# Kernel tuning notes

Hardware: AMD Instinct MI355X
Metric: run time of the kernel (lower is better)

The kernel has to match this reference:

```python
import jax, jax.numpy as jnp
import numpy as np

B, S, R, H = 32, 512, 49, 768


def setup_inputs() -> dict:
    key = jax.random.key(0)
    ks = jax.random.split(key, 32)
    rn = lambda i, shape, s=1.0: jax.random.normal(ks[i], shape, dtype=jnp.float32) * s
    W = 0.05  # weight init scale to keep tanh/softmax in a sane range
    return {
        'text_features': rn(0, (B, S, H)),
        'img_features': rn(1, (B, R, H)),
        't1_w': rn(2, (H, H), W), 't1_b': rn(3, (H,), W),
        'i1_w': rn(4, (H, H), W),
        'a1_w': rn(5, (2 * H,), W), 'a1_b': rn(6, (), W),
        't2_w': rn(7, (H, H), W),
        'i2_w': rn(8, (H, H), W), 'i2_b': rn(9, (H,), W),
        'a2_w': rn(10, (2 * H,), W), 'a2_b': rn(11, (), W),
        'gt_w': rn(12, (H, H), W), 'gt_b': rn(13, (H,), W),
        'gi_w': rn(14, (H, H), W), 'gi_b': rn(15, (H,), W),
        'gg_w': rn(16, (2 * H, 1), W), 'gg_b': rn(17, (1,), W),
        'ft_w': rn(18, (H, H), W),
        'fm_w': rn(19, (H, H), W), 'fm_b': rn(20, (H,), W),
        'fg_w': rn(21, (2 * H, 1), W), 'fg_b': rn(22, (1,), W),
        'fr_w': rn(23, (H, H), W), 'fr_b': rn(24, (H,), W),
    }


def reference(text_features, img_features, t1_w, t1_b, i1_w, a1_w, a1_b,
              t2_w, i2_w, i2_b, a2_w, a2_b, gt_w, gt_b, gi_w, gi_b,
              gg_w, gg_b, ft_w, fm_w, fm_b, fg_w, fg_b, fr_w, fr_b):
    H = text_features.shape[-1]
    # --- CoAttention, stage 1 (text attends over image regions) ---
    # tanh(concat) is elementwise and att_linear_1 is rank-1, so split the score:
    # score[b,s,r] = tanh(t1(x_s)) . a1[:H] + tanh(i1(y_r)) . a1[H:] + b
    t_sc = jnp.tanh(text_features @ t1_w + t1_b) @ a1_w[:H]          # (B,S)
    i_sc = jnp.tanh(img_features @ i1_w) @ a1_w[H:]                  # (B,R)
    visual_att = jax.nn.softmax(t_sc[:, :, None] + i_sc[:, None, :] + a1_b, axis=-1)  # (B,S,R)
    att_img = jnp.einsum('bsr,brh->bsh', visual_att, img_features)   # (B,S,H)
    # --- CoAttention, stage 2 (attended-image queries attend over text) ---
    # concat order is [img, text] -> a2[:H] pairs with img part
    q_sc = jnp.tanh(att_img @ i2_w + i2_b) @ a2_w[:H]                # (B,S)
    k_sc = jnp.tanh(text_features @ t2_w) @ a2_w[H:]                 # (B,S)
    textual_att = jax.nn.softmax(q_sc[:, :, None] + k_sc[:, None, :] + a2_b, axis=-1)  # (B,S,S)
    att_text = jnp.einsum('bij,bjh->bih', textual_att, text_features)  # (B,S,H)
    # --- GMF gated fusion ---
    new_img = jnp.tanh(att_img @ gi_w + gi_b)
    new_txt = jnp.tanh(att_text @ gt_w + gt_b)
    gate = jax.nn.sigmoid(jnp.concatenate([new_img, new_txt], axis=-1) @ gg_w + gg_b)  # (B,S,1)
    multimodal = gate * new_img + (1.0 - gate) * new_txt
    # --- filtration gate ---
    concat_feat = jnp.concatenate([text_features @ ft_w, multimodal @ fm_w + fm_b], axis=-1)
    fgate = jax.nn.sigmoid(concat_feat @ fg_w + fg_b)                # (B,S,1)
    return fgate * jnp.tanh(multimodal @ fr_w + fr_b)
```

## Files before the change

### kernel.cpp

```cpp
#include <hip/hip_runtime.h>
#include <hip/hip_bf16.h>
#include <math.h>

constexpr int BD = 32;
constexpr int SD = 512;
constexpr int RD = 49;
constexpr int HD = 768;
constexpr int MT = BD * SD;
constexpr int MI = BD * RD;
constexpr int NP = 6;
constexpr int MBT3 = MT / 256;
constexpr int MBI3 = 7;
constexpr int NB3 = 3;
constexpr int NWG3 = (MBT3 + MBI3) * NB3;
constexpr int NT3 = HD / 64;

typedef __bf16 bf16;
typedef __bf16 bf16x4 __attribute__((ext_vector_type(4)));
typedef __bf16 bf16x8 __attribute__((ext_vector_type(8)));
typedef float f32x4 __attribute__((ext_vector_type(4)));

#define GLOAD_LDS16(g, l) __builtin_amdgcn_global_load_lds( \
    (__attribute__((address_space(1))) void*)(g),           \
    (__attribute__((address_space(3))) void*)(l), 16, 0, 0)
#define BAR() __builtin_amdgcn_s_barrier()
#define SCHED_FENCE() __builtin_amdgcn_sched_barrier(0)
#define WAITV(n) asm volatile("s_waitcnt vmcnt(" #n ")" ::: "memory")

__device__ __forceinline__ float fast_tanh(float x) {
    const float e = __expf(2.f * x);
    return 1.f - 2.f / (e + 1.f);
}

__global__ __launch_bounds__(256) void prep_text(
    const float* __restrict__ text, const float* __restrict__ v_f,
    bf16* __restrict__ text_bf, float* __restrict__ s_txt)
{
    const int row = blockIdx.x * 4 + (threadIdx.x >> 6);
    const int lane = threadIdx.x & 63;
    const float* tr = text + (size_t)row * HD;
    bf16* tb = text_bf + (size_t)row * HD;
    float acc = 0.f;
    #pragma unroll
    for (int c = 0; c < 3; ++c) {
        const int o = c * 256 + lane * 4;
        const f32x4 x = *(const f32x4*)(tr + o);
        const f32x4 v = *(const f32x4*)(v_f + o);
        bf16x4 b; b[0] = (bf16)x[0]; b[1] = (bf16)x[1]; b[2] = (bf16)x[2]; b[3] = (bf16)x[3];
        *(bf16x4*)(tb + o) = b;
        acc += x[0] * v[0] + x[1] * v[1] + x[2] * v[2] + x[3] * v[3];
    }
    for (int off = 32; off; off >>= 1) acc += __shfl_xor(acc, off);
    if (lane == 0) s_txt[row] = acc;
}

__global__ __launch_bounds__(256) void prep_misc(
    const float* __restrict__ ft_w, const float* __restrict__ fm_w,
    const float* __restrict__ fm_b, const float* __restrict__ fg_w,
    float* __restrict__ v_f, float* __restrict__ v_m, float* __restrict__ c_m,
    const float* __restrict__ img, bf16* __restrict__ img_bf,
    const float* __restrict__ t2_w, const float* __restrict__ i1_w,
    bf16* __restrict__ wt_t, bf16* __restrict__ wt_i)
{
    __shared__ float tile[64][65];
    const int bid = blockIdx.x;
    if (bid < 385) {
        const int idx = bid * 4 + (threadIdx.x >> 6);
        const int lane = threadIdx.x & 63;
        const float* row; const float* vecp; float* outp;
        if (idx < HD)            { row = ft_w + (size_t)idx * HD;        vecp = fg_w;      outp = v_f + idx; }
        else if (idx < 2 * HD)   { row = fm_w + (size_t)(idx - HD) * HD; vecp = fg_w + HD; outp = v_m + (idx - HD); }
        else if (idx == 2 * HD)  { row = fm_b;                           vecp = fg_w + HD; outp = c_m; }
        else return;
        float acc = 0.f;
        #pragma unroll
        for (int i = 0; i < HD / 64; ++i) acc += row[lane + 64 * i] * vecp[lane + 64 * i];
        for (int off = 32; off; off >>= 1) acc += __shfl_xor(acc, off);
        if (lane == 0) *outp = acc;
    } else if (bid < 385 + 588) {
        const int i = (bid - 385) * 256 + threadIdx.x;
        const int n8 = BD * RD * HD / 8;
        if (i >= n8) return;
        const size_t o = (size_t)i * 8;
        const f32x4 x0 = *(const f32x4*)(img + o);
        const f32x4 x1 = *(const f32x4*)(img + o + 4);
        bf16x8 b;
        b[0]=(bf16)x0[0]; b[1]=(bf16)x0[1]; b[2]=(bf16)x0[2]; b[3]=(bf16)x0[3];
        b[4]=(bf16)x1[0]; b[5]=(bf16)x1[1]; b[6]=(bf16)x1[2]; b[7]=(bf16)x1[3];
        *(bf16x8*)(img_bf + o) = b;
    } else {
        const int idx2 = bid - (385 + 588);
        const int z = idx2 / 144, rem = idx2 % 144;
        const int bx = rem % 12, by = rem / 12;
        const float* W = z ? i1_w : t2_w;
        bf16* Wt = z ? wt_i : wt_t;
        const int k0 = bx * 64, n0 = by * 64;
        const int t = threadIdx.x;
        const int rb = t >> 6, c = t & 63;
        #pragma unroll
        for (int i = 0; i < 16; ++i) {
            const int r = rb + i * 4;
            tile[r][c] = W[(size_t)(k0 + r) * HD + n0 + c];
        }
        __syncthreads();
        #pragma unroll
        for (int i = 0; i < 16; ++i) {
            const int r = rb + i * 4;
            Wt[(size_t)(n0 + r) * HD + k0 + c] = (bf16)tile[c][r];
        }
    }
}

__global__ __launch_bounds__(512, 2) void gemm3(
    const bf16* __restrict__ Atext, const bf16* __restrict__ WtT,
    const float* __restrict__ vecT, float* __restrict__ partT,
    const bf16* __restrict__ Aimg, const bf16* __restrict__ WtI,
    const float* __restrict__ vecI, float* __restrict__ partI)
{
    __shared__ __align__(16) bf16 As[2 * 16384];
    __shared__ __align__(16) bf16 Bs[2 * 16384];

    const int bid = blockIdx.x;
    const int q = NWG3 / 8, r = NWG3 % 8;
    const int xcd = bid % 8, sidx = bid / 8;
    const int o = (xcd < r ? xcd * (q + 1) : r * (q + 1) + (xcd - r) * q) + sidx;
    const int mb = o / NB3, nb = o % NB3;

    const bool isT = mb < MBT3;
    const bf16* A    = isT ? Atext : Aimg;
    const bf16* Wt   = isT ? WtT : WtI;
    const float* vec = isT ? vecT : vecI;
    float* part      = isT ? partT : partI;
    const int m0 = (isT ? mb : mb - MBT3) * 256;
    const int n0 = nb * 256;

    const int t = threadIdx.x;
    const int w = t >> 6, lane = t & 63;
    const int quad = lane >> 4, l16 = lane & 15;
    const int wm_idx = w & 3, wn_idx = w >> 2;
    const int wm2 = wm_idx * 64, wn2 = wn_idx * 128;

    const bf16* Ag = A  + (size_t)(m0 + l16) * HD + quad * 8;
    const bf16* Bg = Wt + (size_t)(n0 + l16) * HD + quad * 8;

    f32x4 acc[4][8] = {};

#define STAGE3(tt, bb) {                                                     \
    const int kk = (tt) * 64;                                                \
    _Pragma("unroll")                                                        \
    for (int h = 0; h < 2; ++h) {                                            \
        _Pragma("unroll")                                                    \
        for (int j = 0; j < 2; ++j) {                                        \
            const int rc = 2 * w + j;                                        \
            GLOAD_LDS16(Ag + (size_t)rc * 16 * HD + kk + h * 32,             \
                        As + (bb) * 16384 + (h * 16 + rc) * 512);            \
            GLOAD_LDS16(Bg + (size_t)rc * 16 * HD + kk + h * 32,             \
                        Bs + (bb) * 16384 + (h * 16 + rc) * 512);            \
        }                                                                    \
    }                                                                        \
}

#define COMPUTE3(bb) {                                                       \
    _Pragma("unroll")                                                        \
    for (int h = 0; h < 2; ++h) {                                            \
        bf16x8 af[4], bg[8];                                                 \
        _Pragma("unroll")                                                    \
        for (int fi = 0; fi < 4; ++fi)                                       \
            af[fi] = *(const bf16x8*)(As + (bb) * 16384 +                    \
                       (h * 16 + wm_idx * 4 + fi) * 512 + lane * 8);         \
        _Pragma("unroll")                                                    \
        for (int fj = 0; fj < 8; ++fj)                                       \
            bg[fj] = *(const bf16x8*)(Bs + (bb) * 16384 +                    \
                       (h * 16 + wn_idx * 8 + fj) * 512 + lane * 8);         \
        _Pragma("unroll")                                                    \
        for (int fi = 0; fi < 4; ++fi)                                       \
            _Pragma("unroll")                                                \
            for (int fj = 0; fj < 8; ++fj)                                   \
                acc[fi][fj] = __builtin_amdgcn_mfma_f32_16x16x32_bf16(       \
                    af[fi], bg[fj], acc[fi][fj], 0, 0, 0);                   \
    }                                                                        \
}

    STAGE3(0, 0);
    for (int tt = 0; tt < NT3 - 1; ++tt) {
        STAGE3(tt + 1, (tt + 1) & 1);
        WAITV(8);
        BAR();
        SCHED_FENCE();
        COMPUTE3(tt & 1);
        SCHED_FENCE();
        BAR();
    }
    WAITV(0);
    BAR();
    SCHED_FENCE();
    COMPUTE3((NT3 - 1) & 1);

#undef STAGE3
#undef COMPUTE3

    float vv[8];
    #pragma unroll
    for (int fj = 0; fj < 8; ++fj) vv[fj] = vec[n0 + wn2 + fj * 16 + l16];

    #pragma unroll
    for (int fi = 0; fi < 4; ++fi) {
        #pragma unroll
        for (int reg = 0; reg < 4; ++reg) {
            float p = 0.f;
            #pragma unroll
            for (int fj = 0; fj < 8; ++fj)
                p += fast_tanh(acc[fi][fj][reg]) * vv[fj];
            p += __shfl_xor(p, 1);
            p += __shfl_xor(p, 2);
            p += __shfl_xor(p, 4);
            p += __shfl_xor(p, 8);
            if (l16 == 0) {
                const int row = m0 + wm2 + fi * 16 + quad * 4 + reg;
                part[(size_t)row * NP + nb * 2 + wn_idx] = p;
            }
        }
    }
}

__global__ __launch_bounds__(256) void wsum3(
    const float* __restrict__ k_part, const float* __restrict__ i_part,
    const bf16* __restrict__ text_bf, const float* __restrict__ img,
    float* __restrict__ at_part, float* __restrict__ aimg)
{
    __shared__ float S[SD];
    __shared__ float red[4];
    __shared__ float P2[2][96][8];
    const int bid = blockIdx.x;
    const int t = threadIdx.x;

    if (bid < 128) {
        const int b = bid >> 2, jq = bid & 3;
        for (int j = t; j < SD; j += 256) {
            const float* p = k_part + (size_t)(b * SD + j) * NP;
            S[j] = p[0] + p[1] + p[2] + p[3] + p[4] + p[5];
        }
        __syncthreads();
        float m = fmaxf(S[t], S[t + 256]);
        for (int off = 32; off; off >>= 1) m = fmaxf(m, __shfl_xor(m, off));
        if ((t & 63) == 0) red[t >> 6] = m;
        __syncthreads();
        m = fmaxf(fmaxf(red[0], red[1]), fmaxf(red[2], red[3]));
        const float e0 = __expf(S[t] - m), e1 = __expf(S[t + 256] - m);
        S[t] = e0; S[t + 256] = e1;
        float lsum = e0 + e1;
        for (int off = 32; off; off >>= 1) lsum += __shfl_xor(lsum, off);
        __syncthreads();
        if ((t & 63) == 0) red[t >> 6] = lsum;
        __syncthreads();
        const float inv = 1.f / (red[0] + red[1] + red[2] + red[3]);
        const int o = t % 96, jh = t / 96;
        if (jh < 2) {
            float a[8] = {};
            const bf16* Xb = text_bf + ((size_t)b * SD + jq * 128 + jh * 64) * HD + o * 8;
            const float* Sp = S + jq * 128 + jh * 64;
            #pragma unroll 8
            for (int jj = 0; jj < 64; ++jj) {
                const bf16x8 v = *(const bf16x8*)(Xb + (size_t)jj * HD);
                const float s = Sp[jj];
                #pragma unroll
                for (int e = 0; e < 8; ++e) a[e] += s * (float)v[e];
            }
            #pragma unroll
            for (int e = 0; e < 8; ++e) P2[jh][o][e] = a[e];
        }
        __syncthreads();
        if (t < 96) {
            float* dst = at_part + ((size_t)(b * 4 + jq)) * HD + t * 8;
            f32x4 o0, o1;
            #pragma unroll
            for (int e = 0; e < 4; ++e) o0[e] = (P2[0][t][e] + P2[1][t][e]) * inv;
            #pragma unroll
            for (int e = 0; e < 4; ++e) o1[e] = (P2[0][t][e + 4] + P2[1][t][e + 4]) * inv;
            *(f32x4*)dst = o0;
            *(f32x4*)(dst + 4) = o1;
        }
    } else {
        const int idx = bid - 128;
        const int b = idx & 31, hy = idx >> 5;
        if (t < 64) {
            float s0 = -1e30f;
            if (t < RD) {
                const float* p = i_part + (size_t)(b * RD + t) * NP;
                s0 = p[0] + p[1] + p[2] + p[3] + p[4] + p[5];
            }
            float m = s0;
            for (int off = 32; off; off >>= 1) m = fmaxf(m, __shfl_xor(m, off));
            float e = (t < RD) ? __expf(s0 - m) : 0.f;
            float lsum = e;
            for (int off = 32; off; off >>= 1) lsum += __shfl_xor(lsum, off);
            if (t < RD) S[t] = e;
            if (t == 0) red[0] = 1.f / lsum;
        }
        __syncthreads();
        const float inv = red[0];
        const int h = hy * 256 + t;
        const float* Xb = img + (size_t)b * RD * HD + h;
        float acc = 0.f;
        #pragma unroll 7
        for (int j = 0; j < RD; ++j) acc += S[j] * Xb[(size_t)j * HD];
        aimg[b * HD + h] = acc * inv;
    }
}

__global__ __launch_bounds__(256) void ni_nt3(
    const float* __restrict__ aimg, const float* __restrict__ at_part,
    const float* __restrict__ gi_w, const float* __restrict__ gi_b,
    const float* __restrict__ gt_w, const float* __restrict__ gt_b,
    float* __restrict__ ni, float* __restrict__ nt)
{
    const int b = blockIdx.x, n0 = blockIdx.y * 128, which = blockIdx.z;
    const float* W = which ? gt_w : gi_w;
    const float* bias = which ? gt_b : gi_b;
    float* Y = which ? nt : ni;

    __shared__ float Xs[HD];
    __shared__ float part[8][32][4];
    const int t = threadIdx.x;
    if (which) {
        for (int h = t; h < HD; h += 256)
            Xs[h] = at_part[((size_t)(b * 4 + 0)) * HD + h] + at_part[((size_t)(b * 4 + 1)) * HD + h]
                  + at_part[((size_t)(b * 4 + 2)) * HD + h] + at_part[((size_t)(b * 4 + 3)) * HD + h];
    } else {
        for (int h = t; h < HD; h += 256) Xs[h] = aimg[b * HD + h];
    }
    __syncthreads();
    const int lane32 = t & 31, kq = t >> 5;
    const int n = n0 + lane32 * 4;
    f32x4 acc = {0.f, 0.f, 0.f, 0.f};
    const float* Wp = W + (size_t)(kq * 96) * HD + n;
    #pragma unroll 4
    for (int k = 0; k < 96; ++k) {
        const f32x4 wv = *(const f32x4*)(Wp + (size_t)k * HD);
        const float x = Xs[kq * 96 + k];
        acc[0] += x * wv[0]; acc[1] += x * wv[1];
        acc[2] += x * wv[2]; acc[3] += x * wv[3];
    }
    *(f32x4*)&part[kq][lane32][0] = acc;
    __syncthreads();
    if (t < 128) {
        float s = 0.f;
        #pragma unroll
        for (int q2 = 0; q2 < 8; ++q2) s += part[q2][t >> 2][t & 3];
        Y[b * HD + n0 + t] = fast_tanh(s + bias[n0 + t]);
    }
}

__global__ __launch_bounds__(256) void gateT3(
    const float* __restrict__ ni, const float* __restrict__ nt,
    const float* __restrict__ gg_w, const float* __restrict__ gg_b,
    const float* __restrict__ v_m, const float* __restrict__ c_m,
    const float* __restrict__ fg_b,
    const float* __restrict__ fr_w, const float* __restrict__ fr_b,
    float* __restrict__ T, float* __restrict__ s_mm)
{
    const int b = blockIdx.x, n0 = blockIdx.y * 128, t = threadIdx.x;
    __shared__ float Mm[HD];
    __shared__ float part[8][32][4];
    __shared__ float red[4];
    __shared__ float gsh;

    float accg = 0.f;
    for (int n = t; n < HD; n += 256)
        accg += ni[b * HD + n] * gg_w[n] + nt[b * HD + n] * gg_w[HD + n];
    for (int off = 32; off; off >>= 1) accg += __shfl_xor(accg, off);
    if ((t & 63) == 0) red[t >> 6] = accg;
    __syncthreads();
    if (t == 0) gsh = 1.f / (1.f + expf(-(red[0] + red[1] + red[2] + red[3] + gg_b[0])));
    __syncthreads();
    const float g = gsh;
    float a2 = 0.f;
    for (int n = t; n < HD; n += 256) {
        const float m = g * ni[b * HD + n] + (1.f - g) * nt[b * HD + n];
        Mm[n] = m;
        a2 += m * v_m[n];
    }
    __syncthreads();
    const int lane32 = t & 31, kq = t >> 5;
    const int n = n0 + lane32 * 4;
    f32x4 acc = {0.f, 0.f, 0.f, 0.f};
    const float* Wp = fr_w + (size_t)(kq * 96) * HD + n;
    #pragma unroll 4
    for (int k = 0; k < 96; ++k) {
        const f32x4 wv = *(const f32x4*)(Wp + (size_t)k * HD);
        const float x = Mm[kq * 96 + k];
        acc[0] += x * wv[0]; acc[1] += x * wv[1];
        acc[2] += x * wv[2]; acc[3] += x * wv[3];
    }
    *(f32x4*)&part[kq][lane32][0] = acc;
    if (blockIdx.y == 0) {
        for (int off = 32; off; off >>= 1) a2 += __shfl_xor(a2, off);
        if ((t & 63) == 0) red[t >> 6] = a2;
    }
    __syncthreads();
    if (blockIdx.y == 0 && t == 0)
        s_mm[b] = red[0] + red[1] + red[2] + red[3] + *c_m + fg_b[0];
    if (t < 128) {
        float s = 0.f;
        #pragma unroll
        for (int q2 = 0; q2 < 8; ++q2) s += part[q2][t >> 2][t & 3];
        T[b * HD + n0 + t] = fast_tanh(s + fr_b[n0 + t]);
    }
}

__global__ __launch_bounds__(256) void out_kernel(const float* __restrict__ s_txt,
                                                  const float* __restrict__ s_mm,
                                                  const float* __restrict__ T,
                                                  float* __restrict__ out) {
    const size_t idx = ((size_t)blockIdx.x * 256 + threadIdx.x) * 4;
    const int h = (int)(idx % HD);
    const int bs = (int)(idx / HD);
    const int b = bs >> 9;
    float f = s_txt[bs] + s_mm[b];
    f = 1.f / (1.f + expf(-f));
    const float* Tp = T + b * HD + h;
    f32x4 o;
    o[0] = f * Tp[0]; o[1] = f * Tp[1]; o[2] = f * Tp[2]; o[3] = f * Tp[3];
    *(f32x4*)(out + idx) = o;
}

extern "C" void kernel_launch(void* const* d_in, const int* in_sizes, int n_in,
                              void* d_out, int out_size, void* d_ws, size_t ws_size,
                              hipStream_t stream) {
    const float* text = (const float*)d_in[0];
    const float* img  = (const float*)d_in[1];
    const float* i1_w = (const float*)d_in[4];
    const float* a1_w = (const float*)d_in[5];
    const float* t2_w = (const float*)d_in[7];
    const float* a2_w = (const float*)d_in[10];
    const float* gt_w = (const float*)d_in[12];
    const float* gt_b = (const float*)d_in[13];
    const float* gi_w = (const float*)d_in[14];
    const float* gi_b = (const float*)d_in[15];
    const float* gg_w = (const float*)d_in[16];
    const float* gg_b = (const float*)d_in[17];
    const float* ft_w = (const float*)d_in[18];
    const float* fm_w = (const float*)d_in[19];
    const float* fm_b = (const float*)d_in[20];
    const float* fg_w = (const float*)d_in[21];
    const float* fg_b = (const float*)d_in[22];
    const float* fr_w = (const float*)d_in[23];
    const float* fr_b = (const float*)d_in[24];
    float* out = (float*)d_out;

    float* sc_ = out;
    float* i_part  = sc_;
    float* k_part  = sc_ + 38400;
    float* aimg    = sc_ + 449600;
    float* v_f     = sc_ + 498752;
    float* v_m     = sc_ + 499520;
    float* c_m     = sc_ + 500288;
    float* at_part = sc_ + 500352;
    float* ni      = sc_ + 598656;
    float* nt      = sc_ + 623232;
    bf16* text_bf  = (bf16*)(sc_ + 672384);
    bf16* img_bf   = (bf16*)(sc_ + 6963840);
    bf16* wt_t     = (bf16*)(sc_ + 7565952);
    bf16* wt_i     = (bf16*)(sc_ + 7860864);

    float* ws    = (float*)d_ws;
    float* s_txt = ws;
    float* s_mm  = ws + 16384;
    float* T     = ws + 16448;

    prep_misc<<<dim3(385 + 588 + 288), dim3(256), 0, stream>>>(
        ft_w, fm_w, fm_b, fg_w, v_f, v_m, c_m, img, img_bf, t2_w, i1_w, wt_t, wt_i);
    prep_text<<<dim3(MT / 4), dim3(256), 0, stream>>>(text, v_f, text_bf, s_txt);
    gemm3<<<dim3(NWG3), dim3(512), 0, stream>>>(
        text_bf, wt_t, a2_w + HD, k_part, img_bf, wt_i, a1_w + HD, i_part);
    wsum3<<<dim3(224), dim3(256), 0, stream>>>(
        k_part, i_part, text_bf, img, at_part, aimg);
    ni_nt3<<<dim3(BD, 6, 2), dim3(256), 0, stream>>>(
        aimg, at_part, gi_w, gi_b, gt_w, gt_b, ni, nt);
    gateT3<<<dim3(BD, 6), dim3(256), 0, stream>>>(
        ni, nt, gg_w, gg_b, v_m, c_m, fg_b, fr_w, fr_b, T, s_mm);
    out_kernel<<<dim3((MT * HD / 4) / 256), dim3(256), 0, stream>>>(s_txt, s_mm, T, out);
}
```

Baseline: 252.6 us.

## Fuse tail kernels into one cooperative kernel with grid-wide syncs

Replaces the four tail launches (weighted sums, gated projections, gate/fr projection, output broadcast) with a single cooperative kernel of 448 workgroups separated by grid.sync barriers. The aim is to remove per-launch overhead and the idle gaps between small dependent kernels. In exchange, the final 50 MB output write now runs through a grid-stride loop over fewer workgroups, and grid syncs add their own latency. Early phases leave most workgroups idle.

Result: slower. 425.4 us (+68.4%).

```diff
diff --git a/kernel.cpp b/kernel.cpp
--- a/kernel.cpp
+++ b/kernel.cpp
@@ -1,6 +1,9 @@
 #include <hip/hip_runtime.h>
 #include <hip/hip_bf16.h>
+#include <hip/hip_cooperative_groups.h>
 #include <math.h>
+
+namespace cg = cooperative_groups;
 
 constexpr int BD = 32;
 constexpr int SD = 512;
@@ -14,6 +17,7 @@
 constexpr int NB3 = 3;
 constexpr int NWG3 = (MBT3 + MBI3) * NB3;
 constexpr int NT3 = HD / 64;
+constexpr int TWG = 448;
 
 typedef __bf16 bf16;
 typedef __bf16 bf16x4 __attribute__((ext_vector_type(4)));
@@ -223,21 +227,35 @@
     }
 }
 
-__global__ __launch_bounds__(256) void wsum3(
-    const float* __restrict__ k_part, const float* __restrict__ i_part,
-    const bf16* __restrict__ text_bf, const float* __restrict__ img,
-    float* __restrict__ at_part, float* __restrict__ aimg)
+struct TailArgs {
+    const float* k_part; const float* i_part;
+    const bf16* text_bf; const float* img;
+    float* at_part; float* aimg;
+    const float* gi_w; const float* gi_b; const float* gt_w; const float* gt_b;
+    float* ni; float* nt;
+    const float* gg_w; const float* gg_b; const float* v_m; const float* c_m;
+    const float* fg_b; const float* fr_w; const float* fr_b;
+    float* T; float* s_mm;
+    const float* s_txt; float* out;
+};
+
+__global__ __launch_bounds__(256) void tail_fused(TailArgs a)
 {
     __shared__ float S[SD];
     __shared__ float red[4];
     __shared__ float P2[2][96][8];
-    const int bid = blockIdx.x;
+    __shared__ float Xs[HD];
+    __shared__ float part8[8][32][4];
+    __shared__ float gsh;
+
+    cg::grid_group grid = cg::this_grid();
+    const int blk = blockIdx.x;
     const int t = threadIdx.x;
 
-    if (bid < 128) {
-        const int b = bid >> 2, jq = bid & 3;
+    if (blk < 128) {
+        const int b = blk >> 2, jq = blk & 3;
         for (int j = t; j < SD; j += 256) {
-            const float* p = k_part + (size_t)(b * SD + j) * NP;
+            const float* p = a.k_part + (size_t)(b * SD + j) * NP;
             S[j] = p[0] + p[1] + p[2] + p[3] + p[4] + p[5];
         }
         __syncthreads();
@@ -256,22 +274,22 @@
         const float inv = 1.f / (red[0] + red[1] + red[2] + red[3]);
         const int o = t % 96, jh = t / 96;
         if (jh < 2) {
-            float a[8] = {};
-            const bf16* Xb = text_bf + ((size_t)b * SD + jq * 128 + jh * 64) * HD + o * 8;
+            float acc[8] = {};
+            const bf16* Xb = a.text_bf + ((size_t)b * SD + jq * 128 + jh * 64) * HD + o * 8;
             const float* Sp = S + jq * 128 + jh * 64;
             #pragma unroll 8
             for (int jj = 0; jj < 64; ++jj) {
                 const bf16x8 v = *(const bf16x8*)(Xb + (size_t)jj * HD);
                 const float s = Sp[jj];
                 #pragma unroll
-                for (int e = 0; e < 8; ++e) a[e] += s * (float)v[e];
+                for (int e = 0; e < 8; ++e) acc[e] += s * (float)v[e];
             }
             #pragma unroll
-            for (int e = 0; e < 8; ++e) P2[jh][o][e] = a[e];
+            for (int e = 0; e < 8; ++e) P2[jh][o][e] = acc[e];
         }
         __syncthreads();
         if (t < 96) {
-            float* dst = at_part + ((size_t)(b * 4 + jq)) * HD + t * 8;
+            float* dst = a.at_part + ((size_t)(b * 4 + jq)) * HD + t * 8;
             f32x4 o0, o1;
             #pragma unroll
             for (int e = 0; e < 4; ++e) o0[e] = (P2[0][t][e] + P2[1][t][e]) * inv;
@@ -280,13 +298,13 @@
             *(f32x4*)dst = o0;
             *(f32x4*)(dst + 4) = o1;
         }
-    } else {
-        const int idx = bid - 128;
+    } else if (blk < 224) {
+        const int idx = blk - 128;
         const int b = idx & 31, hy = idx >> 5;
         if (t < 64) {
             float s0 = -1e30f;
             if (t < RD) {
-                const float* p = i_part + (size_t)(b * RD + t) * NP;
+                const float* p = a.i_part + (size_t)(b * RD + t) * NP;
                 s0 = p[0] + p[1] + p[2] + p[3] + p[4] + p[5];
             }
             float m = s0;
@@ -300,128 +318,117 @@
         __syncthreads();
         const float inv = red[0];
         const int h = hy * 256 + t;
-        const float* Xb = img + (size_t)b * RD * HD + h;
+        const float* Xb = a.img + (size_t)b * RD * HD + h;
         float acc = 0.f;
         #pragma unroll 7
         for (int j = 0; j < RD; ++j) acc += S[j] * Xb[(size_t)j * HD];
-        aimg[b * HD + h] = acc * inv;
-    }
-}
-
-__global__ __launch_bounds__(256) void ni_nt3(
-    const float* __restrict__ aimg, const float* __restrict__ at_part,
-    const float* __restrict__ gi_w, const float* __restrict__ gi_b,
-    const float* __restrict__ gt_w, const float* __restrict__ gt_b,
-    float* __restrict__ ni, float* __restrict__ nt)
-{
-    const int b = blockIdx.x, n0 = blockIdx.y * 128, which = blockIdx.z;
-    const float* W = which ? gt_w : gi_w;
-    const float* bias = which ? gt_b : gi_b;
-    float* Y = which ? nt : ni;
-
-    __shared__ float Xs[HD];
-    __shared__ float part[8][32][4];
-    const int t = threadIdx.x;
-    if (which) {
-        for (int h = t; h < HD; h += 256)
-            Xs[h] = at_part[((size_t)(b * 4 + 0)) * HD + h] + at_part[((size_t)(b * 4 + 1)) * HD + h]
-                  + at_part[((size_t)(b * 4 + 2)) * HD + h] + at_part[((size_t)(b * 4 + 3)) * HD + h];
-    } else {
-        for (int h = t; h < HD; h += 256) Xs[h] = aimg[b * HD + h];
-    }
-    __syncthreads();
-    const int lane32 = t & 31, kq = t >> 5;
-    const int n = n0 + lane32 * 4;
-    f32x4 acc = {0.f, 0.f, 0.f, 0.f};
-    const float* Wp = W + (size_t)(kq * 96) * HD + n;
-    #pragma unroll 4
-    for (int k = 0; k < 96; ++k) {
-        const f32x4 wv = *(const f32x4*)(Wp + (size_t)k * HD);
-        const float x = Xs[kq * 96 + k];
-        acc[0] += x * wv[0]; acc[1] += x * wv[1];
-        acc[2] += x * wv[2]; acc[3] += x * wv[3];
-    }
-    *(f32x4*)&part[kq][lane32][0] = acc;
-    __syncthreads();
-    if (t < 128) {
-        float s = 0.f;
-        #pragma unroll
-        for (int q2 = 0; q2 < 8; ++q2) s += part[q2][t >> 2][t & 3];
-        Y[b * HD + n0 + t] = fast_tanh(s + bias[n0 + t]);
-    }
-}
-
-__global__ __launch_bounds__(256) void gateT3(
-    const float* __restrict__ ni, const float* __restrict__ nt,
-    const float* __restrict__ gg_w, const float* __restrict__ gg_b,
-    const float* __restrict__ v_m, const float* __restrict__ c_m,
-    const float* __restrict__ fg_b,
-    const float* __restrict__ fr_w, const float* __restrict__ fr_b,
-    float* __restrict__ T, float* __restrict__ s_mm)
-{
-    const int b = blockIdx.x, n0 = blockIdx.y * 128, t = threadIdx.x;
-    __shared__ float Mm[HD];
-    __shared__ float part[8][32][4];
-    __shared__ float red[4];
-    __shared__ float gsh;
-
-    float accg = 0.f;
-    for (int n = t; n < HD; n += 256)
-        accg += ni[b * HD + n] * gg_w[n] + nt[b * HD + n] * gg_w[HD + n];
-    for (int off = 32; off; off >>= 1) accg += __shfl_xor(accg, off);
-    if ((t & 63) == 0) red[t >> 6] = accg;
-    __syncthreads();
-    if (t == 0) gsh = 1.f / (1.f + expf(-(red[0] + red[1] + red[2] + red[3] + gg_b[0])));
-    __syncthreads();
-    const float g = gsh;
-    float a2 = 0.f;
-    for (int n = t; n < HD; n += 256) {
-        const float m = g * ni[b * HD + n] + (1.f - g) * nt[b * HD + n];
-        Mm[n] = m;
-        a2 += m * v_m[n];
-    }
-    __syncthreads();
-    const int lane32 = t & 31, kq = t >> 5;
-    const int n = n0 + lane32 * 4;
-    f32x4 acc = {0.f, 0.f, 0.f, 0.f};
-    const float* Wp = fr_w + (size_t)(kq * 96) * HD + n;
-    #pragma unroll 4
-    for (int k = 0; k < 96; ++k) {
-        const f32x4 wv = *(const f32x4*)(Wp + (size_t)k * HD);
-        const float x = Mm[kq * 96 + k];
-        acc[0] += x * wv[0]; acc[1] += x * wv[1];
-        acc[2] += x * wv[2]; acc[3] += x * wv[3];
-    }
-    *(f32x4*)&part[kq][lane32][0] = acc;
-    if (blockIdx.y == 0) {
-        for (int off = 32; off; off >>= 1) a2 += __shfl_xor(a2, off);
-        if ((t & 63) == 0) red[t >> 6] = a2;
-    }
-    __syncthreads();
-    if (blockIdx.y == 0 && t == 0)
-        s_mm[b] = red[0] + red[1] + red[2] + red[3] + *c_m + fg_b[0];
-    if (t < 128) {
-        float s = 0.f;
-        #pragma unroll
-        for (int q2 = 0; q2 < 8; ++q2) s += part[q2][t >> 2][t & 3];
-        T[b * HD + n0 + t] = fast_tanh(s + fr_b[n0 + t]);
-    }
-}
-
-__global__ __launch_bounds__(256) void out_kernel(const float* __restrict__ s_txt,
-                                                  const float* __restrict__ s_mm,
-                                                  const float* __restrict__ T,
-                                                  float* __restrict__ out) {
-    const size_t idx = ((size_t)blockIdx.x * 256 + threadIdx.x) * 4;
-    const int h = (int)(idx % HD);
-    const int bs = (int)(idx / HD);
-    const int b = bs >> 9;
-    float f = s_txt[bs] + s_mm[b];
-    f = 1.f / (1.f + expf(-f));
-    const float* Tp = T + b * HD + h;
-    f32x4 o;
-    o[0] = f * Tp[0]; o[1] = f * Tp[1]; o[2] = f * Tp[2]; o[3] = f * Tp[3];
-    *(f32x4*)(out + idx) = o;
+        a.aimg[b * HD + h] = acc * inv;
+    }
+
+    grid.sync();
+
+    if (blk < 384) {
+        const int which = blk / 192;
+        const int rem = blk % 192;
+        const int b = rem / 6, ny = rem % 6;
+        const int n0 = ny * 128;
+        const float* W = which ? a.gt_w : a.gi_w;
+        const float* bias = which ? a.gt_b : a.gi_b;
+        float* Y = which ? a.nt : a.ni;
+
+        if (which) {
+            for (int h = t; h < HD; h += 256)
+                Xs[h] = a.at_part[((size_t)(b * 4 + 0)) * HD + h] + a.at_part[((size_t)(b * 4 + 1)) * HD + h]
+                      + a.at_part[((size_t)(b * 4 + 2)) * HD + h] + a.at_part[((size_t)(b * 4 + 3)) * HD + h];
+        } else {
+            for (int h = t; h < HD; h += 256) Xs[h] = a.aimg[b * HD + h];
+        }
+        __syncthreads();
+        const int lane32 = t & 31, kq = t >> 5;
+        const int n = n0 + lane32 * 4;
+        f32x4 acc = {0.f, 0.f, 0.f, 0.f};
+        const float* Wp = W + (size_t)(kq * 96) * HD + n;
+        #pragma unroll 4
+        for (int k = 0; k < 96; ++k) {
+            const f32x4 wv = *(const f32x4*)(Wp + (size_t)k * HD);
+            const float x = Xs[kq * 96 + k];
+            acc[0] += x * wv[0]; acc[1] += x * wv[1];
+            acc[2] += x * wv[2]; acc[3] += x * wv[3];
+        }
+        *(f32x4*)&part8[kq][lane32][0] = acc;
+        __syncthreads();
+        if (t < 128) {
+            float s = 0.f;
+            #pragma unroll
+            for (int q2 = 0; q2 < 8; ++q2) s += part8[q2][t >> 2][t & 3];
+            Y[b * HD + n0 + t] = fast_tanh(s + bias[n0 + t]);
+        }
+    }
+
+    grid.sync();
+
+    if (blk < 192) {
+        const int b = blk / 6, ny = blk % 6;
+        const int n0 = ny * 128;
+
+        float accg = 0.f;
+        for (int n = t; n < HD; n += 256)
+            accg += a.ni[b * HD + n] * a.gg_w[n] + a.nt[b * HD + n] * a.gg_w[HD + n];
+        for (int off = 32; off; off >>= 1) accg += __shfl_xor(accg, off);
+        if ((t & 63) == 0) red[t >> 6] = accg;
+        __syncthreads();
+        if (t == 0) gsh = 1.f / (1.f + expf(-(red[0] + red[1] + red[2] + red[3] + a.gg_b[0])));
+        __syncthreads();
+        const float g = gsh;
+        float a2 = 0.f;
+        for (int n = t; n < HD; n += 256) {
+            const float m = g * a.ni[b * HD + n] + (1.f - g) * a.nt[b * HD + n];
+            Xs[n] = m;
+            a2 += m * a.v_m[n];
+        }
+        __syncthreads();
+        const int lane32 = t & 31, kq = t >> 5;
+        const int n = n0 + lane32 * 4;
+        f32x4 acc = {0.f, 0.f, 0.f, 0.f};
+        const float* Wp = a.fr_w + (size_t)(kq * 96) * HD + n;
+        #pragma unroll 4
+        for (int k = 0; k < 96; ++k) {
+            const f32x4 wv = *(const f32x4*)(Wp + (size_t)k * HD);
+            const float x = Xs[kq * 96 + k];
+            acc[0] += x * wv[0]; acc[1] += x * wv[1];
+            acc[2] += x * wv[2]; acc[3] += x * wv[3];
+        }
+        *(f32x4*)&part8[kq][lane32][0] = acc;
+        if (ny == 0) {
+            for (int off = 32; off; off >>= 1) a2 += __shfl_xor(a2, off);
+            if ((t & 63) == 0) red[t >> 6] = a2;
+        }
+        __syncthreads();
+        if (ny == 0 && t == 0)
+            a.s_mm[b] = red[0] + red[1] + red[2] + red[3] + *a.c_m + a.fg_b[0];
+        if (t < 128) {
+            float s = 0.f;
+            #pragma unroll
+            for (int q2 = 0; q2 < 8; ++q2) s += part8[q2][t >> 2][t & 3];
+            a.T[b * HD + n0 + t] = fast_tanh(s + a.fr_b[n0 + t]);
+        }
+    }
+
+    grid.sync();
+
+    const size_t total4 = (size_t)MT * HD / 4;
+    for (size_t i = (size_t)blk * 256 + t; i < total4; i += (size_t)TWG * 256) {
+        const size_t idx = i * 4;
+        const int h = (int)(idx % HD);
+        const int bs = (int)(idx / HD);
+        const int b = bs >> 9;
+        float f = a.s_txt[bs] + a.s_mm[b];
+        f = 1.f / (1.f + expf(-f));
+        const float* Tp = a.T + b * HD + h;
+        f32x4 o;
+        o[0] = f * Tp[0]; o[1] = f * Tp[1]; o[2] = f * Tp[2]; o[3] = f * Tp[3];
+        *(f32x4*)(a.out + idx) = o;
+    }
 }
 
 extern "C" void kernel_launch(void* const* d_in, const int* in_sizes, int n_in,
@@ -473,11 +480,17 @@
     prep_text<<<dim3(MT / 4), dim3(256), 0, stream>>>(text, v_f, text_bf, s_txt);
     gemm3<<<dim3(NWG3), dim3(512), 0, stream>>>(
         text_bf, wt_t, a2_w + HD, k_part, img_bf, wt_i, a1_w + HD, i_part);
-    wsum3<<<dim3(224), dim3(256), 0, stream>>>(
-        k_part, i_part, text_bf, img, at_part, aimg);
-    ni_nt3<<<dim3(BD, 6, 2), dim3(256), 0, stream>>>(
-        aimg, at_part, gi_w, gi_b, gt_w, gt_b, ni, nt);
-    gateT3<<<dim3(BD, 6), dim3(256), 0, stream>>>(
-        ni, nt, gg_w, gg_b, v_m, c_m, fg_b, fr_w, fr_b, T, s_mm);
-    out_kernel<<<dim3((MT * HD / 4) / 256), dim3(256), 0, stream>>>(s_txt, s_mm, T, out);
-}
+    TailArgs ta;
+    ta.k_part = k_part; ta.i_part = i_part;
+    ta.text_bf = text_bf; ta.img = img;
+    ta.at_part = at_part; ta.aimg = aimg;
+    ta.gi_w = gi_w; ta.gi_b = gi_b; ta.gt_w = gt_w; ta.gt_b = gt_b;
+    ta.ni = ni; ta.nt = nt;
+    ta.gg_w = gg_w; ta.gg_b = gg_b; ta.v_m = v_m; ta.c_m = c_m;
+    ta.fg_b = fg_b; ta.fr_w = fr_w; ta.fr_b = fr_b;
+    ta.T = T; ta.s_mm = s_mm;
+    ta.s_txt = s_txt; ta.out = out;
+    void* kargs[] = { (void*)&ta };
+    hipLaunchCooperativeKernel((const void*)tail_fused, dim3(TWG), dim3(256),
+                               kargs, 0, stream);
+}
```
